# Kernel tuning notes

Hardware: AMD Instinct MI355X
Metric: run time of the kernel (lower is better)

## Reference

```python
import jax, jax.numpy as jnp
import numpy as np

B, S, D, H = 2, 4096, 1024, 16
HD = D // H  # 64


def setup_inputs() -> dict:
    key = jax.random.key(0)
    ks = jax.random.split(key, 9)
    init = lambda k, shape: (jax.random.normal(k, shape, dtype=jnp.float32) * 0.02)
    return {
        "x": jax.random.normal(ks[0], (B, S, D), dtype=jnp.float32),
        "Wq": init(ks[1], (D, D)), "bq": init(ks[2], (D,)),
        "Wk": init(ks[3], (D, D)), "bk": init(ks[4], (D,)),
        "Wv": init(ks[5], (D, D)), "bv": init(ks[6], (D,)),
        "Wo": init(ks[7], (D, D)), "bo": init(ks[8], (D,)),
    }


def _split_heads(t):
    # [B, S, D] -> [B, H, S, HD]
    b, s, d = t.shape
    return t.reshape(b, s, H, HD).transpose(0, 2, 1, 3)


def reference(x, Wq, bq, Wk, bk, Wv, bv, Wo, bo):
    # q/k/v projections (torch Linear: x @ W.T + b)
    q = _split_heads(x @ Wq.T + bq)
    k = _split_heads(x @ Wk.T + bk)
    v = _split_heads(x @ Wv.T + bv)
    scale = 1.0 / np.sqrt(HD).astype(np.float32)
    # chunked_attention uses full K/V per chunk => equivalent to full attention.
    scores = jnp.einsum("bhqd,bhkd->bhqk", q, k) * scale
    # softmax computed in fp32 then cast back (matches F.softmax(dtype=float32))
    attn = jax.nn.softmax(scores.astype(jnp.float32), axis=-1).astype(scores.dtype)
    out = jnp.einsum("bhqk,bhkd->bhqd", attn, v)
    out = out.transpose(0, 2, 1, 3).reshape(B, S, D)  # combine heads
    return out @ Wo.T + bo
```

## Files before the change

kernel.cpp:

```cpp
#include <hip/hip_runtime.h>
#include <hip/hip_bf16.h>
#include <stdint.h>

typedef __attribute__((ext_vector_type(8))) short short8;
typedef __attribute__((ext_vector_type(4))) short short4v;
typedef __attribute__((ext_vector_type(4))) float f32x4;

#define MFMA16(A, B, C) __builtin_amdgcn_mfma_f32_16x16x32_bf16(A, B, C, 0, 0, 0)

#define GLDS16(gp, lp) __builtin_amdgcn_global_load_lds(                     \
    (const __attribute__((address_space(1))) unsigned int*)(gp),             \
    (__attribute__((address_space(3))) unsigned int*)(lp), 16, 0, 0)

static constexpr int kS  = 4096;
static constexpr int kD  = 1024;
static constexpr int kH  = 16;
static constexpr int kHD = 64;

__device__ __forceinline__ short bf16_bits(float f) {
    __hip_bfloat16 h = __float2bfloat16(f);
    return *(short*)&h;
}

__device__ __forceinline__ unsigned int pk_bf16(float a, float b) {
    __hip_bfloat162 h = __float22bfloat162_rn(make_float2(a, b));
    return *(unsigned int*)&h;
}

__device__ __forceinline__ short8 cvt8(const float* __restrict__ p) {
    f32x4 a = ((const f32x4*)p)[0];
    f32x4 b = ((const f32x4*)p)[1];
    short8 r;
    r[0] = bf16_bits(a[0]); r[1] = bf16_bits(a[1]);
    r[2] = bf16_bits(a[2]); r[3] = bf16_bits(a[3]);
    r[4] = bf16_bits(b[0]); r[5] = bf16_bits(b[1]);
    r[6] = bf16_bits(b[2]); r[7] = bf16_bits(b[3]);
    return r;
}

__device__ __forceinline__ unsigned char f32_to_e4m3(float f) {
    unsigned int u = __float_as_uint(f);
    unsigned int s = (u >> 24) & 0x80u;
    unsigned int a = u & 0x7fffffffu;
    if (a < 0x3c800000u) {
        float af = __uint_as_float(a);
        unsigned int sub = (unsigned int)(af * 512.0f + 0.5f);
        return (unsigned char)(s | sub);
    }
    unsigned int r = a + 0x80000u;
    unsigned int m = (r >> 20) & 7u;
    int eb = (int)(r >> 23) - 127 + 7;
    unsigned int bits = ((unsigned int)eb << 3) | m;
    if (bits > 0x7Eu) bits = 0x7Eu;
    return (unsigned char)(s | bits);
}
__device__ __forceinline__ float e4m3_to_f32(unsigned int b) {
    unsigned int s = b & 0x80u;
    unsigned int e = (b >> 3) & 15u;
    unsigned int m = b & 7u;
    float f = e ? __uint_as_float(((e + 120u) << 23) | (m << 20))
                : (float)m * 0.001953125f;
    return s ? -f : f;
}

__global__ __launch_bounds__(256) void cvt_f32_bf16(
    const float* __restrict__ src, __hip_bfloat16* __restrict__ dst)
{
    const int i = blockIdx.x * 256 + threadIdx.x;
    f32x4 v = ((const f32x4*)src)[i];
    short4v o;
    o[0] = bf16_bits(v[0]); o[1] = bf16_bits(v[1]);
    o[2] = bf16_bits(v[2]); o[3] = bf16_bits(v[3]);
    ((short4v*)dst)[i] = o;
}

__global__ __launch_bounds__(256) void cvt_w4(
    const float* __restrict__ w0, const float* __restrict__ w1,
    const float* __restrict__ w2, const float* __restrict__ w3,
    __hip_bfloat16* __restrict__ dst)
{
    const int blk = blockIdx.x;
    const int sel = blk >> 10;
    const float* src = sel == 0 ? w0 : sel == 1 ? w1 : sel == 2 ? w2 : w3;
    const int i = (blk & 1023) * 256 + threadIdx.x;
    f32x4 v = ((const f32x4*)src)[i];
    short4v o;
    o[0] = bf16_bits(v[0]); o[1] = bf16_bits(v[1]);
    o[2] = bf16_bits(v[2]); o[3] = bf16_bits(v[3]);
    ((short4v*)(dst + (size_t)sel * kD * kD))[i] = o;
}


__global__ __launch_bounds__(256) void gemm_qkv(
    const __hip_bfloat16* __restrict__ X, const __hip_bfloat16* __restrict__ Wb,
    const float* __restrict__ bq, const float* __restrict__ bk,
    const float* __restrict__ bv,
    __hip_bfloat16* __restrict__ Qw, __hip_bfloat16* __restrict__ Kw,
    __hip_bfloat16* __restrict__ Vtw)
{
    __shared__ short As[128 * 64];
    __shared__ short Bs[128 * 64];

    const int lane = threadIdx.x & 63, wave = threadIdx.x >> 6;
    const int quad = lane >> 4, l16 = lane & 15;
    const int sel = blockIdx.y >> 3;
    const int m0 = blockIdx.x * 128, n0 = (blockIdx.y & 7) * 128;
    const int wm = wave & 1, wn = wave >> 1;

    const float* bias = sel == 0 ? bq : sel == 1 ? bk : bv;
    const short* Xg = (const short*)X + (size_t)m0 * kD;
    const short* Wg = (const short*)Wb + (size_t)sel * kD * kD + (size_t)n0 * kD;

    f32x4 acc[4][4];
    #pragma unroll
    for (int mt = 0; mt < 4; ++mt)
        #pragma unroll
        for (int nt = 0; nt < 4; ++nt) acc[mt][nt] = f32x4{0.f, 0.f, 0.f, 0.f};

    const int srow = lane >> 3;
    const int gch  = (lane & 7) ^ srow;

    for (int k0 = 0; k0 < kD; k0 += 64) {
        __syncthreads();
        #pragma unroll
        for (int i = 0; i < 4; ++i) {
            const int rowbase = wave * 32 + i * 8;
            const int row = rowbase + srow;
            GLDS16(Xg + (size_t)row * kD + k0 + gch * 8, &As[rowbase * 64]);
            GLDS16(Wg + (size_t)row * kD + k0 + gch * 8, &Bs[rowbase * 64]);
        }
        __syncthreads();

        #pragma unroll
        for (int c = 0; c < 2; ++c) {
            short8 af[4], bf[4];
            const int rx = l16 & 7;
            #pragma unroll
            for (int mt = 0; mt < 4; ++mt)
                af[mt] = *(const short8*)&As[(wm * 64 + mt * 16 + l16) * 64
                                             + (((c * 4 + quad) ^ rx) * 8)];
            #pragma unroll
            for (int nt = 0; nt < 4; ++nt)
                bf[nt] = *(const short8*)&Bs[(wn * 64 + nt * 16 + l16) * 64
                                             + (((c * 4 + quad) ^ rx) * 8)];
            #pragma unroll
            for (int mt = 0; mt < 4; ++mt)
                #pragma unroll
                for (int nt = 0; nt < 4; ++nt)
                    acc[mt][nt] = MFMA16(af[mt], bf[nt], acc[mt][nt]);
        }
    }

    #pragma unroll
    for (int nt = 0; nt < 4; ++nt) {
        const int n = n0 + wn * 64 + nt * 16 + l16;
        const float bvv = bias[n];
        #pragma unroll
        for (int mt = 0; mt < 4; ++mt) {
            if (sel == 2) {
                const int m = m0 + wm * 64 + mt * 16 + quad * 4;
                short4v pk;
                #pragma unroll
                for (int r = 0; r < 4; ++r)
                    pk[r] = bf16_bits(acc[mt][nt][r] + bvv);
                const int bh2 = (m >> 12) * kH + (n >> 6);
                short* dst = (short*)Vtw
                    + ((size_t)bh2 * kHD + (size_t)(n & (kHD - 1))) * kS
                    + (size_t)(m & (kS - 1));
                *(short4v*)dst = pk;
            } else {
                __hip_bfloat16* dst = sel == 0 ? Qw : Kw;
                const float scale = sel == 0 ? 0.18033688f : 1.0f;
                #pragma unroll
                for (int r = 0; r < 4; ++r) {
                    const int m = m0 + wm * 64 + mt * 16 + quad * 4 + r;
                    const float v = (acc[mt][nt][r] + bvv) * scale;
                    const size_t addr = (((size_t)(m >> 12) * kH + (n >> 6)) * kS
                                         + (size_t)(m & (kS - 1))) * kHD
                                        + (size_t)(n & (kHD - 1));
                    dst[addr] = __float2bfloat16(v);
                }
            }
        }
    }
}

__global__ __launch_bounds__(256) void gemm_out(
    const __hip_bfloat16* __restrict__ X, const __hip_bfloat16* __restrict__ W,
    const float* __restrict__ bias, float* __restrict__ out)
{
    __shared__ short As[128 * 64];
    __shared__ short Bs[128 * 64];

    const int lane = threadIdx.x & 63, wave = threadIdx.x >> 6;
    const int quad = lane >> 4, l16 = lane & 15;
    const int m0 = blockIdx.x * 128, n0 = blockIdx.y * 128;
    const int wm = wave & 1, wn = wave >> 1;

    const short* Xg = (const short*)X + (size_t)m0 * kD;
    const short* Wg = (const short*)W + (size_t)n0 * kD;

    f32x4 acc[4][4];
    #pragma unroll
    for (int mt = 0; mt < 4; ++mt)
        #pragma unroll
        for (int nt = 0; nt < 4; ++nt) acc[mt][nt] = f32x4{0.f, 0.f, 0.f, 0.f};

    const int srow = lane >> 3;
    const int gch  = (lane & 7) ^ srow;

    for (int k0 = 0; k0 < kD; k0 += 64) {
        __syncthreads();
        #pragma unroll
        for (int i = 0; i < 4; ++i) {
            const int rowbase = wave * 32 + i * 8;
            const int row = rowbase + srow;
            GLDS16(Xg + (size_t)row * kD + k0 + gch * 8, &As[rowbase * 64]);
            GLDS16(Wg + (size_t)row * kD + k0 + gch * 8, &Bs[rowbase * 64]);
        }
        __syncthreads();

        #pragma unroll
        for (int c = 0; c < 2; ++c) {
            short8 af[4], bf[4];
            const int rx = l16 & 7;
            #pragma unroll
            for (int mt = 0; mt < 4; ++mt)
                af[mt] = *(const short8*)&As[(wm * 64 + mt * 16 + l16) * 64
                                             + (((c * 4 + quad) ^ rx) * 8)];
            #pragma unroll
            for (int nt = 0; nt < 4; ++nt)
                bf[nt] = *(const short8*)&Bs[(wn * 64 + nt * 16 + l16) * 64
                                             + (((c * 4 + quad) ^ rx) * 8)];
            #pragma unroll
            for (int mt = 0; mt < 4; ++mt)
                #pragma unroll
                for (int nt = 0; nt < 4; ++nt)
                    acc[mt][nt] = MFMA16(af[mt], bf[nt], acc[mt][nt]);
        }
    }

    #pragma unroll
    for (int nt = 0; nt < 4; ++nt) {
        const int n = n0 + wn * 64 + nt * 16 + l16;
        const float bv = bias[n];
        #pragma unroll
        for (int mt = 0; mt < 4; ++mt)
            #pragma unroll
            for (int r = 0; r < 4; ++r) {
                const int m = m0 + wm * 64 + mt * 16 + quad * 4 + r;
                out[(size_t)m * kD + n] = acc[mt][nt][r] + bv;
            }
    }
}

__global__ __launch_bounds__(256, 4) void flash2(
    const __hip_bfloat16* __restrict__ Qw, const __hip_bfloat16* __restrict__ Kw,
    const __hip_bfloat16* __restrict__ Vt, __hip_bfloat16* __restrict__ O)
{
    __shared__ short Ks[2][64 * 64];
    __shared__ short Vs[2][64 * 64];
    __shared__ short Ps[4][32][32];

    const int lane = threadIdx.x & 63, wave = threadIdx.x >> 6;
    const int quad = lane >> 4, l16 = lane & 15;

    const int flat = blockIdx.y * 32 + blockIdx.x;
    const int swz  = (flat & 7) * 128 + (flat >> 3);
    const int bh = swz >> 5, b = bh >> 4, h = bh & 15;
    const int qbase = (swz & 31) * 128 + wave * 32;

    const short* Qg = (const short*)Qw + ((size_t)bh * kS + qbase) * kHD;
    short8 qf[2][2];
    #pragma unroll
    for (int t = 0; t < 2; ++t)
        #pragma unroll
        for (int c = 0; c < 2; ++c)
            qf[t][c] = *(const short8*)(Qg + (t * 16 + l16) * kHD + c * 32 + quad * 8);

    const short* Kg = (const short*)Kw + (size_t)bh * kS * kHD;
    const short* Vg = (const short*)Vt + (size_t)bh * kHD * kS;

    const short ONE = 0x3F80;
    const short8 onesf = {ONE, ONE, ONE, ONE, ONE, ONE, ONE, ONE};

    f32x4 o[2][4], lsumv[2];
    #pragma unroll
    for (int t = 0; t < 2; ++t) {
        lsumv[t] = f32x4{0.f, 0.f, 0.f, 0.f};
        #pragma unroll
        for (int dt = 0; dt < 4; ++dt) o[t][dt] = f32x4{0.f, 0.f, 0.f, 0.f};
    }

    const int srow = lane >> 3;
    const int gch  = (lane & 7) ^ srow;
    const int rx   = l16 & 7;
    const int pswz = (l16 & 3) << 3;

    #pragma unroll
    for (int i = 0; i < 2; ++i) {
        const int rowbase = wave * 16 + i * 8;
        const int row = rowbase + srow;
        GLDS16(Kg + (size_t)row * kHD + gch * 8, &Ks[0][rowbase * 64]);
        GLDS16(Vg + (size_t)row * kS + gch * 8,  &Vs[0][rowbase * 64]);
    }

    for (int k0 = 0; k0 < kS; k0 += 64) {
        const int cur = (k0 >> 6) & 1;
        __syncthreads();
        if (k0 + 64 < kS) {
            const int nxt = cur ^ 1;
            #pragma unroll
            for (int i = 0; i < 2; ++i) {
                const int rowbase = wave * 16 + i * 8;
                const int row = rowbase + srow;
                GLDS16(Kg + (size_t)(k0 + 64 + row) * kHD + gch * 8, &Ks[nxt][rowbase * 64]);
                GLDS16(Vg + (size_t)row * kS + (k0 + 64) + gch * 8,  &Vs[nxt][rowbase * 64]);
            }
        }

        #pragma unroll
        for (int c = 0; c < 2; ++c) {
            #pragma unroll
            for (int kk = 0; kk < 2; ++kk) {
                const int kt = c * 2 + kk;
                const int row = kt * 16 + l16;
                short8 a0 = *(const short8*)&Ks[cur][row * 64 + ((quad ^ rx) * 8)];
                short8 a1 = *(const short8*)&Ks[cur][row * 64 + (((4 + quad) ^ rx) * 8)];
                #pragma unroll
                for (int t = 0; t < 2; ++t) {
                    f32x4 z = {0.f, 0.f, 0.f, 0.f};
                    f32x4 s = MFMA16(a0, qf[t][0], z);
                    s = MFMA16(a1, qf[t][1], s);
                    uint2 pk;
                    pk.x = pk_bf16(__builtin_amdgcn_exp2f(s[0]), __builtin_amdgcn_exp2f(s[1]));
                    pk.y = pk_bf16(__builtin_amdgcn_exp2f(s[2]), __builtin_amdgcn_exp2f(s[3]));
                    *(uint2*)&Ps[wave][t * 16 + l16][(kk * 16 + quad * 4) ^ pswz] = pk;
                }
            }

            short8 pa[2];
            #pragma unroll
            for (int t = 0; t < 2; ++t)
                pa[t] = *(const short8*)&Ps[wave][t * 16 + l16][(quad * 8) ^ pswz];
            __builtin_amdgcn_s_setprio(1);
            #pragma unroll
            for (int t = 0; t < 2; ++t)
                lsumv[t] = MFMA16(pa[t], onesf, lsumv[t]);
            #pragma unroll
            for (int dt = 0; dt < 4; ++dt) {
                const int d = dt * 16 + l16;
                short8 vb = *(const short8*)&Vs[cur][d * 64 + (((c * 4 + quad) ^ rx) * 8)];
                #pragma unroll
                for (int t = 0; t < 2; ++t)
                    o[t][dt] = MFMA16(pa[t], vb, o[t][dt]);
            }
            __builtin_amdgcn_s_setprio(0);
        }
    }

    #pragma unroll
    for (int t = 0; t < 2; ++t)
        #pragma unroll
        for (int r = 0; r < 4; ++r) {
            const float inv = 1.0f / lsumv[t][r];
            const int sq = qbase + t * 16 + quad * 4 + r;
            #pragma unroll
            for (int dt = 0; dt < 4; ++dt)
                O[((size_t)b * kS + sq) * kD + h * kHD + dt * 16 + l16] =
                    __float2bfloat16(o[t][dt][r] * inv);
        }
}

template <bool KV8, bool WB16>
__global__ __launch_bounds__(256) void gemm_kv(
    const float* __restrict__ X, const void* __restrict__ W,
    const float* __restrict__ bias, void* __restrict__ outv)
{
    const int lane = threadIdx.x & 63;
    const int wave = threadIdx.x >> 6;
    const int quad = lane >> 4;
    const int l16  = lane & 15;
    const int m0 = blockIdx.x * 16;
    const int n0 = blockIdx.y * 256 + wave * 64;

    const float* xr = X + (size_t)(m0 + l16) * kD;
    const float* wf = (const float*)W + (size_t)(n0 + l16) * kD;
    const short* wb = (const short*)W + (size_t)(n0 + l16) * kD;

    f32x4 acc[4] = {{0.f,0.f,0.f,0.f},{0.f,0.f,0.f,0.f},
                    {0.f,0.f,0.f,0.f},{0.f,0.f,0.f,0.f}};

    for (int k8 = quad; k8 < kD / 8; k8 += 4) {
        short8 a = cvt8(xr + k8 * 8);
        #pragma unroll
        for (int nt = 0; nt < 4; ++nt) {
            short8 w = WB16 ? *(const short8*)(wb + nt * 16 * kD + k8 * 8)
                            : cvt8(wf + nt * 16 * kD + k8 * 8);
            acc[nt] = MFMA16(a, w, acc[nt]);
        }
    }

    #pragma unroll
    for (int nt = 0; nt < 4; ++nt) {
        const int n = n0 + nt * 16 + l16;
        const float bv = bias[n];
        #pragma unroll
        for (int r = 0; r < 4; ++r) {
            const int m = m0 + quad * 4 + r;
            const float v = acc[nt][r] + bv;
            const size_t addr = (((size_t)(m >> 12) * kH + (n >> 6)) * kS
                                 + (size_t)(m & (kS - 1))) * kHD + (size_t)(n & (kHD - 1));
            if (KV8) ((unsigned char*)outv)[addr] = f32_to_e4m3(v);
            else     ((__hip_bfloat16*)outv)[addr] = __float2bfloat16(v);
        }
    }
}

template <bool KV8, bool WB16>
__global__ __launch_bounds__(256) void flash_fusedq(
    const float* __restrict__ x,  const void* __restrict__ Wq,
    const float* __restrict__ bq, const void* __restrict__ Kw,
    const void* __restrict__ Vw,  __hip_bfloat16* __restrict__ O)
{
    __shared__ short pool[9216];
    __shared__ short Ps[4][32][72];

    const int lane = threadIdx.x & 63;
    const int wave = threadIdx.x >> 6;
    const int quad = lane >> 4;
    const int l16  = lane & 15;
    const int bh   = blockIdx.y;
    const int b    = bh >> 4, h = bh & 15;
    const int qbase = blockIdx.x * 128 + wave * 32;

    {
        const float* xr0 = x + (size_t)(b * kS + qbase + l16) * kD;
        const float* xr1 = xr0 + (size_t)16 * kD;
        const float* wqf = (const float*)Wq + (size_t)(h * kHD + l16) * kD;
        const short* wqb = (const short*)Wq + (size_t)(h * kHD + l16) * kD;
        f32x4 qa[2][4];
        #pragma unroll
        for (int t = 0; t < 2; ++t)
            #pragma unroll
            for (int nt = 0; nt < 4; ++nt) qa[t][nt] = f32x4{0.f,0.f,0.f,0.f};

        for (int k8 = quad; k8 < kD / 8; k8 += 4) {
            short8 a0 = cvt8(xr0 + k8 * 8);
            short8 a1 = cvt8(xr1 + k8 * 8);
            #pragma unroll
            for (int nt = 0; nt < 4; ++nt) {
                short8 w = WB16 ? *(const short8*)(wqb + nt * 16 * kD + k8 * 8)
                                : cvt8(wqf + nt * 16 * kD + k8 * 8);
                qa[0][nt] = MFMA16(a0, w, qa[0][nt]);
                qa[1][nt] = MFMA16(a1, w, qa[1][nt]);
            }
        }
        #pragma unroll
        for (int t = 0; t < 2; ++t)
            #pragma unroll
            for (int nt = 0; nt < 4; ++nt) {
                const float bv = bq[h * kHD + nt * 16 + l16];
                #pragma unroll
                for (int r = 0; r < 4; ++r)
                    pool[wave * 2304 + (t * 16 + quad * 4 + r) * 72 + nt * 16 + l16] =
                        bf16_bits((qa[t][nt][r] + bv) * 0.125f);
            }
    }
    short8 qf[2][2];
    #pragma unroll
    for (int t = 0; t < 2; ++t)
        #pragma unroll
        for (int c = 0; c < 2; ++c)
            qf[t][c] = *(const short8*)&pool[wave * 2304 + (t * 16 + l16) * 72 + c * 32 + quad * 8];

    f32x4 o[2][4];
    float mrow[2][4], lrow[2][4];
    #pragma unroll
    for (int t = 0; t < 2; ++t)
        #pragma unroll
        for (int dt = 0; dt < 4; ++dt) o[t][dt] = f32x4{0.f,0.f,0.f,0.f};
    #pragma unroll
    for (int t = 0; t < 2; ++t)
        #pragma unroll
        for (int r = 0; r < 4; ++r) { mrow[t][r] = -INFINITY; lrow[t][r] = 0.f; }

    const __hip_bfloat16* Kb16 = (const __hip_bfloat16*)Kw + (size_t)bh * kS * kHD;
    const __hip_bfloat16* Vb16 = (const __hip_bfloat16*)Vw + (size_t)bh * kS * kHD;
    const unsigned char*  K8   = (const unsigned char*)Kw + (size_t)bh * kS * kHD;
    const unsigned char*  V8   = (const unsigned char*)Vw + (size_t)bh * kS * kHD;

    for (int k0 = 0; k0 < kS; k0 += 64) {
        __syncthreads();
        #pragma unroll
        for (int i = 0; i < 2; ++i) {
            const int lin = threadIdx.x + i * 256;
            const int kr = lin >> 3, c8 = lin & 7;
            short8 kv, vv;
            if (KV8) {
                uint2 kbits = *(const uint2*)(K8 + (size_t)(k0 + kr) * kHD + c8 * 8);
                uint2 vbits = *(const uint2*)(V8 + (size_t)(k0 + kr) * kHD + c8 * 8);
                #pragma unroll
                for (int j = 0; j < 4; ++j) {
                    kv[j]     = bf16_bits(e4m3_to_f32((kbits.x >> (8 * j)) & 255u));
                    kv[4 + j] = bf16_bits(e4m3_to_f32((kbits.y >> (8 * j)) & 255u));
                    vv[j]     = bf16_bits(e4m3_to_f32((vbits.x >> (8 * j)) & 255u));
                    vv[4 + j] = bf16_bits(e4m3_to_f32((vbits.y >> (8 * j)) & 255u));
                }
            } else {
                kv = *(const short8*)(Kb16 + (size_t)(k0 + kr) * kHD + c8 * 8);
                vv = *(const short8*)(Vb16 + (size_t)(k0 + kr) * kHD + c8 * 8);
            }
            *(short8*)&pool[kr * 72 + c8 * 8] = kv;
            #pragma unroll
            for (int j = 0; j < 8; ++j)
                pool[4608 + (c8 * 8 + j) * 72 + (((kr >> 3) ^ c8) << 3) + (kr & 7)] = vv[j];
        }
        __syncthreads();

        f32x4 sc[2][4];
        #pragma unroll
        for (int kt = 0; kt < 4; ++kt) {
            short8 b0 = *(const short8*)&pool[(kt * 16 + l16) * 72 + quad * 8];
            short8 b1 = *(const short8*)&pool[(kt * 16 + l16) * 72 + 32 + quad * 8];
            f32x4 z = {0.f, 0.f, 0.f, 0.f};
            f32x4 s0 = MFMA16(qf[0][0], b0, z); s0 = MFMA16(qf[0][1], b1, s0);
            f32x4 s1 = MFMA16(qf[1][0], b0, z); s1 = MFMA16(qf[1][1], b1, s1);
            sc[0][kt] = s0; sc[1][kt] = s1;
        }

        #pragma unroll
        for (int t = 0; t < 2; ++t)
            #pragma unroll
            for (int r = 0; r < 4; ++r) {
                float s0 = sc[t][0][r], s1 = sc[t][1][r];
                float s2 = sc[t][2][r], s3 = sc[t][3][r];
                float mx = fmaxf(fmaxf(s0, s1), fmaxf(s2, s3));
                #pragma unroll
                for (int off = 1; off < 16; off <<= 1)
                    mx = fmaxf(mx, __shfl_xor(mx, off, 64));
                const float mnew  = fmaxf(mrow[t][r], mx);
                const float alpha = __builtin_amdgcn_exp2f((mrow[t][r] - mnew) * 1.44269504f);
                mrow[t][r] = mnew;
                const float p0 = __builtin_amdgcn_exp2f((s0 - mnew) * 1.44269504f);
                const float p1 = __builtin_amdgcn_exp2f((s1 - mnew) * 1.44269504f);
                const float p2 = __builtin_amdgcn_exp2f((s2 - mnew) * 1.44269504f);
                const float p3 = __builtin_amdgcn_exp2f((s3 - mnew) * 1.44269504f);
                float ps = (p0 + p1) + (p2 + p3);
                #pragma unroll
                for (int off = 1; off < 16; off <<= 1)
                    ps += __shfl_xor(ps, off, 64);
                lrow[t][r] = lrow[t][r] * alpha + ps;
                o[t][0][r] *= alpha; o[t][1][r] *= alpha;
                o[t][2][r] *= alpha; o[t][3][r] *= alpha;
                const int row = t * 16 + quad * 4 + r;
                Ps[wave][row][l16]      = bf16_bits(p0);
                Ps[wave][row][16 + l16] = bf16_bits(p1);
                Ps[wave][row][32 + l16] = bf16_bits(p2);
                Ps[wave][row][48 + l16] = bf16_bits(p3);
            }

        short8 pa[2][2];
        #pragma unroll
        for (int t = 0; t < 2; ++t)
            #pragma unroll
            for (int c = 0; c < 2; ++c)
                pa[t][c] = *(const short8*)&Ps[wave][t * 16 + l16][c * 32 + quad * 8];
        #pragma unroll
        for (int c = 0; c < 2; ++c)
            #pragma unroll
            for (int dt = 0; dt < 4; ++dt) {
                const int d = dt * 16 + l16;
                short8 vb = *(const short8*)&pool[4608 + d * 72 + ((((c * 4 + quad)) ^ (d >> 3)) << 3)];
                o[0][dt] = MFMA16(pa[0][c], vb, o[0][dt]);
                o[1][dt] = MFMA16(pa[1][c], vb, o[1][dt]);
            }
    }

    #pragma unroll
    for (int t = 0; t < 2; ++t)
        #pragma unroll
        for (int r = 0; r < 4; ++r) {
            const float inv = 1.0f / lrow[t][r];
            const int sq = qbase + t * 16 + quad * 4 + r;
            #pragma unroll
            for (int dt = 0; dt < 4; ++dt)
                O[((size_t)b * kS + sq) * kD + h * kHD + dt * 16 + l16] =
                    __float2bfloat16(o[t][dt][r] * inv);
        }
}

template <bool WB16>
__global__ __launch_bounds__(256) void proj_out(
    const __hip_bfloat16* __restrict__ Xb, const void* __restrict__ W,
    const float* __restrict__ bias, float* __restrict__ out)
{
    const int lane = threadIdx.x & 63;
    const int wave = threadIdx.x >> 6;
    const int quad = lane >> 4;
    const int l16  = lane & 15;
    const int m0 = blockIdx.x * 16;
    const int n0 = blockIdx.y * 256 + wave * 64;

    const short8* xr = (const short8*)((const short*)Xb + (size_t)(m0 + l16) * kD);
    const float*  wf = (const float*)W + (size_t)(n0 + l16) * kD;
    const short*  wb = (const short*)W + (size_t)(n0 + l16) * kD;

    f32x4 acc[4] = {{0.f,0.f,0.f,0.f},{0.f,0.f,0.f,0.f},
                    {0.f,0.f,0.f,0.f},{0.f,0.f,0.f,0.f}};

    for (int k8 = quad; k8 < kD / 8; k8 += 4) {
        short8 a = xr[k8];
        #pragma unroll
        for (int nt = 0; nt < 4; ++nt) {
            short8 w = WB16 ? *(const short8*)(wb + nt * 16 * kD + k8 * 8)
                            : cvt8(wf + nt * 16 * kD + k8 * 8);
            acc[nt] = MFMA16(a, w, acc[nt]);
        }
    }

    #pragma unroll
    for (int nt = 0; nt < 4; ++nt) {
        const int n = n0 + nt * 16 + l16;
        const float bv = bias[n];
        #pragma unroll
        for (int r = 0; r < 4; ++r) {
            const int m = m0 + quad * 4 + r;
            out[(size_t)m * kD + n] = acc[nt][r] + bv;
        }
    }
}

extern "C" void kernel_launch(void* const* d_in, const int* in_sizes, int n_in,
                              void* d_out, int out_size, void* d_ws, size_t ws_size,
                              hipStream_t stream)
{
    const float* x = nullptr;
    const float* Wm[4] = {nullptr, nullptr, nullptr, nullptr};
    const float* bm[4] = {nullptr, nullptr, nullptr, nullptr};
    int wi = 0, bi = 0;
    for (int i = 0; i < n_in; ++i) {
        const int s = in_sizes[i];
        if      (s == 2 * kS * kD)         x = (const float*)d_in[i];
        else if (s == kD * kD && wi < 4)   Wm[wi++] = (const float*)d_in[i];
        else if (s == kD      && bi < 4)   bm[bi++] = (const float*)d_in[i];
    }
    const float *Wq = Wm[0], *Wk = Wm[1], *Wv = Wm[2], *Wo = Wm[3];
    const float *bq = bm[0], *bk = bm[1], *bv = bm[2], *bo = bm[3];
    float* out = (float*)d_out;

    const size_t elems = (size_t)2 * kS * kD;
    const size_t wel   = (size_t)kD * kD;
    const size_t MB = 1024 * 1024;
    dim3 bb(256);

    if (ws_size >= 88 * MB) {
        __hip_bfloat16* xb  = (__hip_bfloat16*)d_ws;
        __hip_bfloat16* Qw  = xb + elems;
        __hip_bfloat16* Kw  = Qw + elems;
        __hip_bfloat16* Vtw = Kw + elems;
        __hip_bfloat16* Ow  = Vtw + elems;
        __hip_bfloat16* Wqb = Ow + elems;
        __hip_bfloat16* Wob = Wqb + 3 * wel;

        cvt_f32_bf16<<<dim3(8192), bb, 0, stream>>>(x, xb);
        cvt_w4<<<dim3(4096), bb, 0, stream>>>(Wq, Wk, Wv, Wo, Wqb);

        gemm_qkv<<<dim3(64, 24), bb, 0, stream>>>(xb, Wqb, bq, bk, bv, Qw, Kw, Vtw);
        flash2<<<dim3(kS / 128, 32), bb, 0, stream>>>(Qw, Kw, Vtw, Ow);
        gemm_out<<<dim3(64, 8), bb, 0, stream>>>(Ow, Wob, bo, out);
        return;
    }

    dim3 gg(512, 4), gf(kS / 128, 2 * kH);
    if (ws_size >= 56 * MB) {
        __hip_bfloat16* Kw  = (__hip_bfloat16*)d_ws;
        __hip_bfloat16* Vw  = Kw + elems;
        __hip_bfloat16* Ow  = Vw + elems;
        __hip_bfloat16* Wqb = Ow + elems;
        __hip_bfloat16* Wkb = Wqb + wel;
        __hip_bfloat16* Wvb = Wkb + wel;
        __hip_bfloat16* Wob = Wvb + wel;
        cvt_w4<<<dim3(4096), bb, 0, stream>>>(Wq, Wk, Wv, Wo, Wqb);
        gemm_kv<false, true><<<gg, bb, 0, stream>>>(x, Wkb, bk, Kw);
        gemm_kv<false, true><<<gg, bb, 0, stream>>>(x, Wvb, bv, Vw);
        flash_fusedq<false, true><<<gf, bb, 0, stream>>>(x, Wqb, bq, Kw, Vw, Ow);
        proj_out<true><<<gg, bb, 0, stream>>>(Ow, Wob, bo, out);
    } else if (ws_size >= 48 * MB) {
        __hip_bfloat16* Kw = (__hip_bfloat16*)d_ws;
        __hip_bfloat16* Vw = Kw + elems;
        __hip_bfloat16* Ow = Vw + elems;
        gemm_kv<false, false><<<gg, bb, 0, stream>>>(x, Wk, bk, Kw);
        gemm_kv<false, false><<<gg, bb, 0, stream>>>(x, Wv, bv, Vw);
        flash_fusedq<false, false><<<gf, bb, 0, stream>>>(x, Wq, bq, Kw, Vw, Ow);
        proj_out<false><<<gg, bb, 0, stream>>>(Ow, Wo, bo, out);
    } else {
        unsigned char* Kw = (unsigned char*)d_ws;
        unsigned char* Vw = Kw + elems;
        __hip_bfloat16* Ow = (__hip_bfloat16*)(Vw + elems);
        gemm_kv<true, false><<<gg, bb, 0, stream>>>(x, Wk, bk, Kw);
        gemm_kv<true, false><<<gg, bb, 0, stream>>>(x, Wv, bv, Vw);
        flash_fusedq<true, false><<<gf, bb, 0, stream>>>(x, Wq, bq, Kw, Vw, Ow);
        proj_out<false><<<gg, bb, 0, stream>>>(Ow, Wo, bo, out);
    }
}
```

Measured before the change: 352.3 us.

## Keep attention probabilities in registers via permlane swaps and fragment-ordered K/V LDS

```diff
diff --git a/kernel.cpp b/kernel.cpp
--- a/kernel.cpp
+++ b/kernel.cpp
@@ -5,6 +5,7 @@
 typedef __attribute__((ext_vector_type(8))) short short8;
 typedef __attribute__((ext_vector_type(4))) short short4v;
 typedef __attribute__((ext_vector_type(4))) float f32x4;
+typedef __attribute__((ext_vector_type(4))) unsigned int uint4v;
 
 #define MFMA16(A, B, C) __builtin_amdgcn_mfma_f32_16x16x32_bf16(A, B, C, 0, 0, 0)
 
@@ -25,6 +26,13 @@
 __device__ __forceinline__ unsigned int pk_bf16(float a, float b) {
     __hip_bfloat162 h = __float22bfloat162_rn(make_float2(a, b));
     return *(unsigned int*)&h;
+}
+
+__device__ __forceinline__ void pl32swap(unsigned int& a, unsigned int& b) {
+    asm volatile("v_permlane32_swap_b32 %0, %1" : "+v"(a), "+v"(b));
+}
+__device__ __forceinline__ void pl16swap(unsigned int& a, unsigned int& b) {
+    asm volatile("v_permlane16_swap_b32 %0, %1" : "+v"(a), "+v"(b));
 }
 
 __device__ __forceinline__ short8 cvt8(const float* __restrict__ p) {
@@ -258,9 +266,8 @@
     const __hip_bfloat16* __restrict__ Qw, const __hip_bfloat16* __restrict__ Kw,
     const __hip_bfloat16* __restrict__ Vt, __hip_bfloat16* __restrict__ O)
 {
-    __shared__ short Ks[2][64 * 64];
-    __shared__ short Vs[2][64 * 64];
-    __shared__ short Ps[4][32][32];
+    __shared__ short Ks[2][8 * 512];
+    __shared__ short Vs[2][8 * 512];
 
     const int lane = threadIdx.x & 63, wave = threadIdx.x >> 6;
     const int quad = lane >> 4, l16 = lane & 15;
@@ -281,28 +288,22 @@
     const short* Kg = (const short*)Kw + (size_t)bh * kS * kHD;
     const short* Vg = (const short*)Vt + (size_t)bh * kHD * kS;
 
-    const short ONE = 0x3F80;
-    const short8 onesf = {ONE, ONE, ONE, ONE, ONE, ONE, ONE, ONE};
-
-    f32x4 o[2][4], lsumv[2];
-    #pragma unroll
-    for (int t = 0; t < 2; ++t) {
-        lsumv[t] = f32x4{0.f, 0.f, 0.f, 0.f};
+    f32x4 o[2][4];
+    float psum[2] = {0.f, 0.f};
+    #pragma unroll
+    for (int t = 0; t < 2; ++t)
         #pragma unroll
         for (int dt = 0; dt < 4; ++dt) o[t][dt] = f32x4{0.f, 0.f, 0.f, 0.f};
-    }
-
-    const int srow = lane >> 3;
-    const int gch  = (lane & 7) ^ srow;
-    const int rx   = l16 & 7;
-    const int pswz = (l16 & 3) << 3;
+
+    const int vdt = ((wave * 2) & 3);
+    const int vc32 = (wave >> 1) * 32;
 
     #pragma unroll
     for (int i = 0; i < 2; ++i) {
-        const int rowbase = wave * 16 + i * 8;
-        const int row = rowbase + srow;
-        GLDS16(Kg + (size_t)row * kHD + gch * 8, &Ks[0][rowbase * 64]);
-        GLDS16(Vg + (size_t)row * kS + gch * 8,  &Vs[0][rowbase * 64]);
+        GLDS16(Kg + (size_t)(wave * 16 + l16) * kHD + i * 32 + quad * 8,
+               &Ks[0][(wave * 2 + i) * 512]);
+        GLDS16(Vg + (size_t)((vdt + i) * 16 + l16) * kS + vc32 + quad * 8,
+               &Vs[0][(wave * 2 + i) * 512]);
     }
 
     for (int k0 = 0; k0 < kS; k0 += 64) {
@@ -312,64 +313,78 @@
             const int nxt = cur ^ 1;
             #pragma unroll
             for (int i = 0; i < 2; ++i) {
-                const int rowbase = wave * 16 + i * 8;
-                const int row = rowbase + srow;
-                GLDS16(Kg + (size_t)(k0 + 64 + row) * kHD + gch * 8, &Ks[nxt][rowbase * 64]);
-                GLDS16(Vg + (size_t)row * kS + (k0 + 64) + gch * 8,  &Vs[nxt][rowbase * 64]);
+                GLDS16(Kg + (size_t)(k0 + 64 + wave * 16 + l16) * kHD + i * 32 + quad * 8,
+                       &Ks[nxt][(wave * 2 + i) * 512]);
+                GLDS16(Vg + (size_t)((vdt + i) * 16 + l16) * kS + (k0 + 64) + vc32 + quad * 8,
+                       &Vs[nxt][(wave * 2 + i) * 512]);
             }
         }
 
         #pragma unroll
         for (int c = 0; c < 2; ++c) {
+            unsigned int X[2][4];
             #pragma unroll
             for (int kk = 0; kk < 2; ++kk) {
                 const int kt = c * 2 + kk;
-                const int row = kt * 16 + l16;
-                short8 a0 = *(const short8*)&Ks[cur][row * 64 + ((quad ^ rx) * 8)];
-                short8 a1 = *(const short8*)&Ks[cur][row * 64 + (((4 + quad) ^ rx) * 8)];
+                short8 a0 = *(const short8*)&Ks[cur][(kt * 2 + 0) * 512 + lane * 8];
+                short8 a1 = *(const short8*)&Ks[cur][(kt * 2 + 1) * 512 + lane * 8];
                 #pragma unroll
                 for (int t = 0; t < 2; ++t) {
                     f32x4 z = {0.f, 0.f, 0.f, 0.f};
                     f32x4 s = MFMA16(a0, qf[t][0], z);
                     s = MFMA16(a1, qf[t][1], s);
-                    uint2 pk;
-                    pk.x = pk_bf16(__builtin_amdgcn_exp2f(s[0]), __builtin_amdgcn_exp2f(s[1]));
-                    pk.y = pk_bf16(__builtin_amdgcn_exp2f(s[2]), __builtin_amdgcn_exp2f(s[3]));
-                    *(uint2*)&Ps[wave][t * 16 + l16][(kk * 16 + quad * 4) ^ pswz] = pk;
+                    const float e0 = __builtin_amdgcn_exp2f(s[0]);
+                    const float e1 = __builtin_amdgcn_exp2f(s[1]);
+                    const float e2 = __builtin_amdgcn_exp2f(s[2]);
+                    const float e3 = __builtin_amdgcn_exp2f(s[3]);
+                    psum[t] += (e0 + e1) + (e2 + e3);
+                    X[t][kk * 2 + 0] = pk_bf16(e0, e1);
+                    X[t][kk * 2 + 1] = pk_bf16(e2, e3);
                 }
             }
 
+            short8 vb[4];
+            #pragma unroll
+            for (int dt = 0; dt < 4; ++dt)
+                vb[dt] = *(const short8*)&Vs[cur][(c * 4 + dt) * 512 + lane * 8];
+
             short8 pa[2];
             #pragma unroll
-            for (int t = 0; t < 2; ++t)
-                pa[t] = *(const short8*)&Ps[wave][t * 16 + l16][(quad * 8) ^ pswz];
+            for (int t = 0; t < 2; ++t) {
+                pl32swap(X[t][0], X[t][2]);
+                pl32swap(X[t][1], X[t][3]);
+                pl16swap(X[t][0], X[t][2]);
+                pl16swap(X[t][1], X[t][3]);
+                uint4v u = {X[t][0], X[t][1], X[t][2], X[t][3]};
+                pa[t] = __builtin_bit_cast(short8, u);
+            }
+
             __builtin_amdgcn_s_setprio(1);
             #pragma unroll
-            for (int t = 0; t < 2; ++t)
-                lsumv[t] = MFMA16(pa[t], onesf, lsumv[t]);
-            #pragma unroll
             for (int dt = 0; dt < 4; ++dt) {
-                const int d = dt * 16 + l16;
-                short8 vb = *(const short8*)&Vs[cur][d * 64 + (((c * 4 + quad) ^ rx) * 8)];
-                #pragma unroll
-                for (int t = 0; t < 2; ++t)
-                    o[t][dt] = MFMA16(pa[t], vb, o[t][dt]);
+                o[0][dt] = MFMA16(pa[0], vb[dt], o[0][dt]);
+                o[1][dt] = MFMA16(pa[1], vb[dt], o[1][dt]);
             }
             __builtin_amdgcn_s_setprio(0);
         }
     }
 
     #pragma unroll
-    for (int t = 0; t < 2; ++t)
+    for (int t = 0; t < 2; ++t) {
+        float L = psum[t];
+        L += __shfl_xor(L, 16, 64);
+        L += __shfl_xor(L, 32, 64);
         #pragma unroll
         for (int r = 0; r < 4; ++r) {
-            const float inv = 1.0f / lsumv[t][r];
+            const float Lr = __shfl(L, quad * 4 + r, 64);
+            const float inv = 1.0f / Lr;
             const int sq = qbase + t * 16 + quad * 4 + r;
             #pragma unroll
             for (int dt = 0; dt < 4; ++dt)
                 O[((size_t)b * kS + sq) * kD + h * kHD + dt * 16 + l16] =
                     __float2bfloat16(o[t][dt][r] * inv);
         }
+    }
 }
 
 template <bool KV8, bool WB16>
```

Result: no change. 358.5 us (+1.8%).

## Keep softmax probabilities in registers by permuting K rows into fragment-ordered LDS

Applied to the files above, without the earlier changes.

```diff
diff --git a/kernel.cpp b/kernel.cpp
--- a/kernel.cpp
+++ b/kernel.cpp
@@ -5,6 +5,7 @@
 typedef __attribute__((ext_vector_type(8))) short short8;
 typedef __attribute__((ext_vector_type(4))) short short4v;
 typedef __attribute__((ext_vector_type(4))) float f32x4;
+typedef __attribute__((ext_vector_type(4))) unsigned int uint4v;
 
 #define MFMA16(A, B, C) __builtin_amdgcn_mfma_f32_16x16x32_bf16(A, B, C, 0, 0, 0)
 
@@ -258,9 +259,8 @@
     const __hip_bfloat16* __restrict__ Qw, const __hip_bfloat16* __restrict__ Kw,
     const __hip_bfloat16* __restrict__ Vt, __hip_bfloat16* __restrict__ O)
 {
-    __shared__ short Ks[2][64 * 64];
-    __shared__ short Vs[2][64 * 64];
-    __shared__ short Ps[4][32][32];
+    __shared__ short Ks[2][8 * 512];
+    __shared__ short Vs[2][8 * 512];
 
     const int lane = threadIdx.x & 63, wave = threadIdx.x >> 6;
     const int quad = lane >> 4, l16 = lane & 15;
@@ -292,68 +292,72 @@
         for (int dt = 0; dt < 4; ++dt) o[t][dt] = f32x4{0.f, 0.f, 0.f, 0.f};
     }
 
-    const int srow = lane >> 3;
-    const int gch  = (lane & 7) ^ srow;
-    const int rx   = l16 & 7;
-    const int pswz = (l16 & 3) << 3;
-
-    #pragma unroll
-    for (int i = 0; i < 2; ++i) {
-        const int rowbase = wave * 16 + i * 8;
-        const int row = rowbase + srow;
-        GLDS16(Kg + (size_t)row * kHD + gch * 8, &Ks[0][rowbase * 64]);
-        GLDS16(Vg + (size_t)row * kS + gch * 8,  &Vs[0][rowbase * 64]);
-    }
+    const int kc = wave >> 1, km = wave & 1;
+    const int krow = kc * 32 + 8 * (l16 >> 2) + 4 * km + (l16 & 3);
+    const short* ka0 = Kg + (size_t)krow * kHD + quad * 8;
+    const short* ka1 = ka0 + 32;
+    const int vdt = (wave & 1) * 2, vc32 = (wave >> 1) * 32;
+    const short* va0 = Vg + (size_t)((vdt + 0) * 16 + l16) * kS + vc32 + quad * 8;
+    const short* va1 = Vg + (size_t)((vdt + 1) * 16 + l16) * kS + vc32 + quad * 8;
+
+    GLDS16(ka0, &Ks[0][(wave * 2 + 0) * 512]);
+    GLDS16(ka1, &Ks[0][(wave * 2 + 1) * 512]);
+    GLDS16(va0, &Vs[0][(wave * 2 + 0) * 512]);
+    GLDS16(va1, &Vs[0][(wave * 2 + 1) * 512]);
+    ka0 += 64 * kHD; ka1 += 64 * kHD; va0 += 64; va1 += 64;
 
     for (int k0 = 0; k0 < kS; k0 += 64) {
         const int cur = (k0 >> 6) & 1;
         __syncthreads();
         if (k0 + 64 < kS) {
             const int nxt = cur ^ 1;
-            #pragma unroll
-            for (int i = 0; i < 2; ++i) {
-                const int rowbase = wave * 16 + i * 8;
-                const int row = rowbase + srow;
-                GLDS16(Kg + (size_t)(k0 + 64 + row) * kHD + gch * 8, &Ks[nxt][rowbase * 64]);
-                GLDS16(Vg + (size_t)row * kS + (k0 + 64) + gch * 8,  &Vs[nxt][rowbase * 64]);
-            }
+            GLDS16(ka0, &Ks[nxt][(wave * 2 + 0) * 512]);
+            GLDS16(ka1, &Ks[nxt][(wave * 2 + 1) * 512]);
+            GLDS16(va0, &Vs[nxt][(wave * 2 + 0) * 512]);
+            GLDS16(va1, &Vs[nxt][(wave * 2 + 1) * 512]);
+            ka0 += 64 * kHD; ka1 += 64 * kHD; va0 += 64; va1 += 64;
         }
 
         #pragma unroll
         for (int c = 0; c < 2; ++c) {
-            #pragma unroll
-            for (int kk = 0; kk < 2; ++kk) {
-                const int kt = c * 2 + kk;
-                const int row = kt * 16 + l16;
-                short8 a0 = *(const short8*)&Ks[cur][row * 64 + ((quad ^ rx) * 8)];
-                short8 a1 = *(const short8*)&Ks[cur][row * 64 + (((4 + quad) ^ rx) * 8)];
+            short8 vb[4];
+            #pragma unroll
+            for (int dt = 0; dt < 4; ++dt)
+                vb[dt] = *(const short8*)&Vs[cur][(c * 4 + dt) * 512 + lane * 8];
+
+            unsigned int P[2][4];
+            #pragma unroll
+            for (int m = 0; m < 2; ++m) {
+                const int fb = c * 4 + m * 2;
+                short8 a0 = *(const short8*)&Ks[cur][(fb + 0) * 512 + lane * 8];
+                short8 a1 = *(const short8*)&Ks[cur][(fb + 1) * 512 + lane * 8];
                 #pragma unroll
                 for (int t = 0; t < 2; ++t) {
                     f32x4 z = {0.f, 0.f, 0.f, 0.f};
                     f32x4 s = MFMA16(a0, qf[t][0], z);
                     s = MFMA16(a1, qf[t][1], s);
-                    uint2 pk;
-                    pk.x = pk_bf16(__builtin_amdgcn_exp2f(s[0]), __builtin_amdgcn_exp2f(s[1]));
-                    pk.y = pk_bf16(__builtin_amdgcn_exp2f(s[2]), __builtin_amdgcn_exp2f(s[3]));
-                    *(uint2*)&Ps[wave][t * 16 + l16][(kk * 16 + quad * 4) ^ pswz] = pk;
+                    P[t][m * 2 + 0] = pk_bf16(__builtin_amdgcn_exp2f(s[0]),
+                                              __builtin_amdgcn_exp2f(s[1]));
+                    P[t][m * 2 + 1] = pk_bf16(__builtin_amdgcn_exp2f(s[2]),
+                                              __builtin_amdgcn_exp2f(s[3]));
                 }
             }
 
             short8 pa[2];
             #pragma unroll
-            for (int t = 0; t < 2; ++t)
-                pa[t] = *(const short8*)&Ps[wave][t * 16 + l16][(quad * 8) ^ pswz];
+            for (int t = 0; t < 2; ++t) {
+                uint4v u = {P[t][0], P[t][1], P[t][2], P[t][3]};
+                pa[t] = __builtin_bit_cast(short8, u);
+            }
+
             __builtin_amdgcn_s_setprio(1);
             #pragma unroll
             for (int t = 0; t < 2; ++t)
                 lsumv[t] = MFMA16(pa[t], onesf, lsumv[t]);
             #pragma unroll
             for (int dt = 0; dt < 4; ++dt) {
-                const int d = dt * 16 + l16;
-                short8 vb = *(const short8*)&Vs[cur][d * 64 + (((c * 4 + quad) ^ rx) * 8)];
-                #pragma unroll
-                for (int t = 0; t < 2; ++t)
-                    o[t][dt] = MFMA16(pa[t], vb, o[t][dt]);
+                o[0][dt] = MFMA16(pa[0], vb[dt], o[0][dt]);
+                o[1][dt] = MFMA16(pa[1], vb[dt], o[1][dt]);
             }
             __builtin_amdgcn_s_setprio(0);
         }
```

After: 344.1 us. 1.02x faster.
